# Optimization experiments

Measured on AMD Instinct MI355X. Metric: run time of the kernel, lower is better.

The kernel has to match this reference:

```python
import jax, jax.numpy as jnp
import numpy as np

HIDDEN = 4096
FFN = 14336
GS = 64  # groupsize


def dequant2(qw, scales, zeros, N):
    """Unpack 2-bit HQQ weights. qw: (N//4, K) int32, scales/zeros: (G, K).
    Returns W of shape (N, K) float: (bits - zeros[n % G]) * scales[n % G]."""
    G = scales.shape[0]
    n = jnp.arange(N)
    packed = qw[n // 4]                      # (N, K)
    shift = ((3 - (n % 4)) * 2).astype(qw.dtype)  # per-row bit shift
    vals = (packed >> shift[:, None]) & 3    # (N, K) 2-bit codes
    g = n % G
    return (vals.astype(scales.dtype) - zeros[g]) * scales[g]


def setup_inputs() -> dict:
    key = jax.random.key(0)
    ks = jax.random.split(key, 12)
    x = jax.random.normal(ks[0], (512, HIDDEN), dtype=jnp.float32)
    qw1 = jax.random.randint(ks[1], (FFN // 4, HIDDEN), 0, 256, dtype=jnp.int32)
    qw3 = jax.random.randint(ks[2], (FFN // 4, HIDDEN), 0, 256, dtype=jnp.int32)
    qw2 = jax.random.randint(ks[3], (HIDDEN // 4, FFN), 0, 256, dtype=jnp.int32)
    G1 = FFN // GS
    G2 = HIDDEN // GS
    s1 = jax.random.uniform(ks[4], (G1, HIDDEN), dtype=jnp.float32) * 0.05
    z1 = jax.random.uniform(ks[5], (G1, HIDDEN), dtype=jnp.float32)
    s3 = jax.random.uniform(ks[6], (G1, HIDDEN), dtype=jnp.float32) * 0.05
    z3 = jax.random.uniform(ks[7], (G1, HIDDEN), dtype=jnp.float32)
    s2 = jax.random.uniform(ks[8], (G2, FFN), dtype=jnp.float32) * 0.05
    z2 = jax.random.uniform(ks[9], (G2, FFN), dtype=jnp.float32)
    return {"x": x, "qw1": qw1, "s1": s1, "z1": z1, "qw3": qw3, "s3": s3,
            "z3": z3, "qw2": qw2, "s2": s2, "z2": z2, "groupsize": GS}


def reference(x, qw1, s1, z1, qw3, s3, z3, qw2, s2, z2, groupsize):
    # gate / up projections: C = x @ W^T, W dequantized to (N, K)
    w1 = dequant2(qw1, s1, z1, FFN)      # (FFN, HIDDEN)
    w3 = dequant2(qw3, s3, z3, FFN)      # (FFN, HIDDEN)
    w2 = dequant2(qw2, s2, z2, HIDDEN)   # (HIDDEN, FFN)
    gate = jnp.einsum('mk,nk->mn', x, w1)   # (M, FFN)
    up = jnp.einsum('mk,nk->mn', x, w3)     # (M, FFN)
    h = jax.nn.silu(gate) * up               # SwiGLU
    out = jnp.einsum('mf,hf->mh', h, w2)     # (M, HIDDEN)
    return out
```

## Files before the change

### kernel.cpp

```cpp
#include <hip/hip_runtime.h>
#include <hip/hip_fp16.h>
#include <stdint.h>

#define HIDDEN 4096
#define FFN    14336
#define MDIM   512
#define G1     224
#define G2     64
#define BK     64
#define KB_H   128
#define KB_F   448

typedef _Float16 f16x8 __attribute__((ext_vector_type(8)));
typedef float f32x4 __attribute__((ext_vector_type(4)));

#define SCHED0() __builtin_amdgcn_sched_barrier(0);
#define LGKM_BAR()                                            \
    asm volatile("s_waitcnt lgkmcnt(0)" ::: "memory");        \
    __builtin_amdgcn_s_barrier();                             \
    __builtin_amdgcn_sched_barrier(0);

__global__ void prep_fused(const float* __restrict__ x,
                           const float* __restrict__ s1, const float* __restrict__ z1,
                           const float* __restrict__ s3, const float* __restrict__ z3,
                           const float* __restrict__ s2, const float* __restrict__ z2,
                           ushort* __restrict__ xbp, uint32_t* __restrict__ szp1,
                           uint32_t* __restrict__ szp3, uint32_t* __restrict__ szp2,
                           float* __restrict__ out) {
    const int b = blockIdx.x, t = threadIdx.x;
    if (b < 1024) {
        int i = b * 256 + t;
        int ls = i & 63;
        int kb = (i >> 6) & (KB_H - 1);
        int mb = i >> 13;
        int row = mb * 16 + (ls & 15);
        int col = kb * 32 + (ls >> 4) * 8;
        const float4* src = (const float4*)&x[(size_t)row * HIDDEN + col];
        float4 v0 = src[0], v1 = src[1];
        __half2 h0 = __floats2half2_rn(v0.x, v0.y);
        __half2 h1 = __floats2half2_rn(v0.z, v0.w);
        __half2 h2 = __floats2half2_rn(v1.x, v1.y);
        __half2 h3 = __floats2half2_rn(v1.z, v1.w);
        ((uint4*)xbp)[i] = make_uint4(
            __builtin_bit_cast(uint32_t, h0), __builtin_bit_cast(uint32_t, h1),
            __builtin_bit_cast(uint32_t, h2), __builtin_bit_cast(uint32_t, h3));
    } else if (b < 6400) {
        const int seg = (b - 1024) / 1792;
        const int i = (b - 1024 - seg * 1792) * 256 + t;
        const float* sp = (seg == 0) ? s1 : (seg == 1) ? s3 : s2;
        const float* zp = (seg == 0) ? z1 : (seg == 1) ? z3 : z2;
        uint32_t* op = (seg == 0) ? szp1 : (seg == 1) ? szp3 : szp2;
        float sv0 = sp[2 * i], sv1 = sp[2 * i + 1];
        float zv0 = zp[2 * i], zv1 = zp[2 * i + 1];
        __half2 hs = __floats2half2_rn(sv0, sv1);
        __half2 hn = __floats2half2_rn(-zv0 * sv0, -zv1 * sv1);
        ((uint2*)op)[i] = make_uint2(__builtin_bit_cast(uint32_t, hs),
                                     __builtin_bit_cast(uint32_t, hn));
    } else {
        int i = (b - 6400) * 256 + t;
        ((float4*)out)[i] = make_float4(0.f, 0.f, 0.f, 0.f);
    }
}

__device__ __forceinline__ uint32_t deq2(uint32_t w0, uint32_t w1, uint32_t sh,
                                         uint32_t spair, uint32_t npair) {
    uint32_t c0 = (w0 >> sh) & 3u;
    uint32_t c1 = (w1 >> sh) & 3u;
    uint32_t sel = 0x01000100u + c0 * 0x0202u + c1 * 0x02020000u;
    uint32_t codes = __builtin_amdgcn_perm(0x42004000u, 0x3C000000u, sel);
    __half2 r = __hfma2(__builtin_bit_cast(__half2, codes),
                        __builtin_bit_cast(__half2, spair),
                        __builtin_bit_cast(__half2, npair));
    return __builtin_bit_cast(uint32_t, r);
}


__global__ __launch_bounds__(256, 2)
void gemm_gateup(const ushort* __restrict__ xbp, const uint32_t* __restrict__ qw1,
                 const uint32_t* __restrict__ sz1, const uint32_t* __restrict__ qw3,
                 const uint32_t* __restrict__ sz3, ushort* __restrict__ hp) {
    __shared__ ushort sB1[2][32 * 64];
    __shared__ ushort sB2[2][32 * 64];
    __shared__ ushort sE[256 * 32];

    const int tid = threadIdx.x;
    const int idx = ((blockIdx.x & 7) * 112) + (blockIdx.x >> 3);
    const int mt = idx & 1, nt = idx >> 1;
    const int m0 = mt * 256, n0 = nt * 32;

    const int lane = tid & 63, w = tid >> 6;
    const int wm = w * 64;
    const int frow = lane & 15, fk = (lane >> 4) * 8;
    const int sw = (frow & 7) << 3;

    uint32_t abase[4];
#pragma unroll
    for (int mi = 0; mi < 4; ++mi)
        abase[mi] = (uint32_t)(((m0 >> 4) + w * 4 + mi) * KB_H) * 512 + lane * 8;

    const int bi = tid & 127;
    const int rp = bi >> 3;
    const int kc = (bi & 7) * 8;
    const int row0 = rp * 2;
    const int g0 = (n0 + row0) % G1;
    const uint32_t* qp = (tid < 128 ? qw1 : qw3) + (size_t)(n0 / 4 + (rp >> 1)) * HIDDEN + kc;
    const uint32_t* zp = (tid < 128 ? sz1 : sz3) + (size_t)g0 * HIDDEN + kc;
    ushort (*sB)[32 * 64] = (tid < 128) ? sB1 : sB2;
    const uint32_t sh0 = 6u - 4u * (uint32_t)(rp & 1);

    f32x4 accG[4][2], accU[4][2];
#pragma unroll
    for (int i = 0; i < 4; ++i)
#pragma unroll
        for (int j = 0; j < 2; ++j) {
            accG[i][j] = (f32x4){0.f, 0.f, 0.f, 0.f};
            accU[i][j] = (f32x4){0.f, 0.f, 0.f, 0.f};
        }

    f16x8 afA[8], afB[8];
    uint4 pwA0, pwA1, pzA0, pzA1, pzA2, pzA3;
    uint4 pwB0, pwB1, pzB0, pzB1, pzB2, pzB3;

#define GU_LDA(AF, tt)                                                         \
    { _Pragma("unroll")                                                        \
      for (int mi = 0; mi < 4; ++mi)                                           \
          _Pragma("unroll")                                                    \
          for (int kk = 0; kk < 2; ++kk)                                       \
              AF[mi * 2 + kk] =                                                \
                  *(const f16x8*)&xbp[abase[mi] + (uint32_t)((tt) * 2 + kk) * 512]; }

#define GU_LD(PW0, PW1, PZ0, PZ1, PZ2, PZ3, k0q)                               \
    PW0 = *(const uint4*)(qp + (k0q));                                         \
    PW1 = *(const uint4*)(qp + (k0q) + 4);                                     \
    PZ0 = *(const uint4*)(zp + (k0q));                                         \
    PZ1 = *(const uint4*)(zp + (k0q) + 4);                                     \
    PZ2 = *(const uint4*)(zp + HIDDEN + (k0q));                                \
    PZ3 = *(const uint4*)(zp + HIDDEN + (k0q) + 4);

#define GU_DEQ(wbuf, PW0, PW1, PZ0, PZ1, PZ2, PZ3)                             \
    { const uint32_t wv[8] = {(PW0).x, (PW0).y, (PW0).z, (PW0).w,              \
                              (PW1).x, (PW1).y, (PW1).z, (PW1).w};             \
      {   const uint32_t sp[4] = {(PZ0).x, (PZ0).z, (PZ1).x, (PZ1).z};         \
          const uint32_t np[4] = {(PZ0).y, (PZ0).w, (PZ1).y, (PZ1).w};         \
          uint32_t o[4];                                                       \
          _Pragma("unroll")                                                    \
          for (int j = 0; j < 4; ++j)                                          \
              o[j] = deq2(wv[2*j], wv[2*j+1], sh0, sp[j], np[j]);              \
          *(uint4*)&sB[wbuf][row0 * 64 + (kc ^ ((row0 & 7) << 3))] =           \
              make_uint4(o[0], o[1], o[2], o[3]);                              \
      }                                                                        \
      {   const uint32_t sp[4] = {(PZ2).x, (PZ2).z, (PZ3).x, (PZ3).z};         \
          const uint32_t np[4] = {(PZ2).y, (PZ2).w, (PZ3).y, (PZ3).w};         \
          uint32_t o[4];                                                       \
          _Pragma("unroll")                                                    \
          for (int j = 0; j < 4; ++j)                                          \
              o[j] = deq2(wv[2*j], wv[2*j+1], sh0 - 2u, sp[j], np[j]);         \
          const int row1 = row0 + 1;                                           \
          *(uint4*)&sB[wbuf][row1 * 64 + (kc ^ ((row1 & 7) << 3))] =           \
              make_uint4(o[0], o[1], o[2], o[3]);                              \
      } }

#define GU_COMP(AF, rbuf)                                                      \
    { _Pragma("unroll")                                                        \
      for (int kk = 0; kk < 2; ++kk) {                                         \
          const int col = ((kk * 32) + fk) ^ sw;                               \
          f16x8 bg0 = *(const f16x8*)&sB1[rbuf][frow * 64 + col];              \
          f16x8 bg1 = *(const f16x8*)&sB1[rbuf][(16 + frow) * 64 + col];       \
          f16x8 bu0 = *(const f16x8*)&sB2[rbuf][frow * 64 + col];              \
          f16x8 bu1 = *(const f16x8*)&sB2[rbuf][(16 + frow) * 64 + col];       \
          _Pragma("unroll")                                                    \
          for (int mi = 0; mi < 4; ++mi) {                                     \
              accG[mi][0] = __builtin_amdgcn_mfma_f32_16x16x32_f16(AF[mi*2+kk], bg0, accG[mi][0], 0, 0, 0); \
              accG[mi][1] = __builtin_amdgcn_mfma_f32_16x16x32_f16(AF[mi*2+kk], bg1, accG[mi][1], 0, 0, 0); \
              accU[mi][0] = __builtin_amdgcn_mfma_f32_16x16x32_f16(AF[mi*2+kk], bu0, accU[mi][0], 0, 0, 0); \
              accU[mi][1] = __builtin_amdgcn_mfma_f32_16x16x32_f16(AF[mi*2+kk], bu1, accU[mi][1], 0, 0, 0); \
          } } }

#define GU_STEP(tcur, AFW, AFR, WBUF, RBUF, PW0, PW1, PZ0, PZ1, PZ2, PZ3, DOLDA, DOLQ) \
    { if (DOLDA) { GU_LDA(AFW, (tcur) + 1) } SCHED0()                          \
      GU_DEQ(WBUF, PW0, PW1, PZ0, PZ1, PZ2, PZ3)                               \
      if (DOLQ) { GU_LD(PW0, PW1, PZ0, PZ1, PZ2, PZ3, ((tcur) + 3) * BK) }     \
      GU_COMP(AFR, RBUF)                                                       \
      LGKM_BAR() }

    GU_LD(pwA0, pwA1, pzA0, pzA1, pzA2, pzA3, 0)
    GU_LDA(afA, 0)
    GU_DEQ(0, pwA0, pwA1, pzA0, pzA1, pzA2, pzA3)
    GU_LD(pwA0, pwA1, pzA0, pzA1, pzA2, pzA3, BK)
    GU_LD(pwB0, pwB1, pzB0, pzB1, pzB2, pzB3, 2 * BK)
    LGKM_BAR()

    for (int t = 0; t < 60; t += 2) {
        GU_STEP(t,     afB, afA, 1, 0, pwA0, pwA1, pzA0, pzA1, pzA2, pzA3, 1, 1)
        GU_STEP(t + 1, afA, afB, 0, 1, pwB0, pwB1, pzB0, pzB1, pzB2, pzB3, 1, 1)
    }
    GU_STEP(60, afB, afA, 1, 0, pwA0, pwA1, pzA0, pzA1, pzA2, pzA3, 1, 1)
    GU_STEP(61, afA, afB, 0, 1, pwB0, pwB1, pzB0, pzB1, pzB2, pzB3, 1, 0)
    GU_STEP(62, afB, afA, 1, 0, pwA0, pwA1, pzA0, pzA1, pzA2, pzA3, 1, 0)
    GU_COMP(afB, 1)

    const int rb = (lane >> 4) * 4, cb = lane & 15;
#pragma unroll
    for (int mi = 0; mi < 4; ++mi)
#pragma unroll
        for (int ni = 0; ni < 2; ++ni) {
            f32x4 g = accG[mi][ni], u = accU[mi][ni];
            const int row = wm + mi * 16 + rb;
            const int colx = ni * 16 + cb;
#pragma unroll
            for (int r = 0; r < 4; ++r) {
                float gv = g[r];
                float hv = __fdividef(gv, 1.0f + __expf(-gv)) * u[r];
                __half hh = __float2half(hv);
                sE[(row + r) * 32 + colx] = __builtin_bit_cast(ushort, hh);
            }
        }
    __syncthreads();
    {
#pragma unroll
        for (int j = 0; j < 4; ++j) {
            const int slot = tid + j * 256;
            const int mbi = slot >> 6, ls = slot & 63;
            uint4 v = *(const uint4*)&sE[(mbi * 16 + (ls & 15)) * 32 + (ls >> 4) * 8];
            *(uint4*)&hp[(size_t)(((m0 >> 4) + mbi) * KB_F + nt) * 512 + ls * 8] = v;
        }
    }
#undef GU_LDA
#undef GU_LD
#undef GU_DEQ
#undef GU_COMP
#undef GU_STEP
}


__global__ __launch_bounds__(256, 2)
void gemm_down(const ushort* __restrict__ hp, const uint32_t* __restrict__ qw2,
               const uint32_t* __restrict__ sz2, float* __restrict__ out) {
    __shared__ ushort sBd[2][32 * 64];

    const int tid = threadIdx.x;
    const int idx = ((blockIdx.x & 7) * 64) + (blockIdx.x >> 3);
    const int mt = idx & 1, nt = (idx >> 1) & 127, sk = idx >> 8;
    const int m0 = mt * 256, n0 = nt * 32;
    const int kb0 = sk * 224;
    const int kbeg = sk * (FFN / 2);

    const int lane = tid & 63, w = tid >> 6;
    const int wm = w * 64;
    const int frow = lane & 15, fk = (lane >> 4) * 8;
    const int sw = (frow & 7) << 3;

    uint32_t abase[4];
#pragma unroll
    for (int mi = 0; mi < 4; ++mi)
        abase[mi] = (uint32_t)(((m0 >> 4) + w * 4 + mi) * KB_F + kb0) * 512 + lane * 8;

    const int r = tid >> 3;
    const int kc = (tid & 7) * 8;
    const int g = ((nt & 1) * 32) + r;
    const uint32_t* qp = qw2 + (size_t)(n0 / 4 + (r >> 2)) * FFN + kbeg + kc;
    const uint32_t* zp = sz2 + (size_t)g * FFN + kbeg + kc;
    const uint32_t sh = 6u - 2u * (uint32_t)(r & 3);

    f32x4 acc[4][2];
#pragma unroll
    for (int i = 0; i < 4; ++i)
#pragma unroll
        for (int j = 0; j < 2; ++j) acc[i][j] = (f32x4){0.f, 0.f, 0.f, 0.f};

    f16x8 afA[8], afB[8];
    uint4 pwA0, pwA1, pzA0, pzA1;
    uint4 pwB0, pwB1, pzB0, pzB1;

#define GD_LDA(AF, tt)                                                         \
    { _Pragma("unroll")                                                        \
      for (int mi = 0; mi < 4; ++mi)                                           \
          _Pragma("unroll")                                                    \
          for (int kk = 0; kk < 2; ++kk)                                       \
              AF[mi * 2 + kk] =                                                \
                  *(const f16x8*)&hp[abase[mi] + (uint32_t)((tt) * 2 + kk) * 512]; }

#define GD_LD(PW0, PW1, PZ0, PZ1, k0q)                                         \
    PW0 = *(const uint4*)(qp + (k0q));                                         \
    PW1 = *(const uint4*)(qp + (k0q) + 4);                                     \
    PZ0 = *(const uint4*)(zp + (k0q));                                         \
    PZ1 = *(const uint4*)(zp + (k0q) + 4);

#define GD_DEQ(wbuf, PW0, PW1, PZ0, PZ1)                                       \
    { const uint32_t wv[8] = {(PW0).x, (PW0).y, (PW0).z, (PW0).w,              \
                              (PW1).x, (PW1).y, (PW1).z, (PW1).w};             \
      const uint32_t sp[4] = {(PZ0).x, (PZ0).z, (PZ1).x, (PZ1).z};             \
      const uint32_t np[4] = {(PZ0).y, (PZ0).w, (PZ1).y, (PZ1).w};             \
      uint32_t o[4];                                                           \
      _Pragma("unroll")                                                        \
      for (int j = 0; j < 4; ++j)                                              \
          o[j] = deq2(wv[2*j], wv[2*j+1], sh, sp[j], np[j]);                   \
      *(uint4*)&sBd[wbuf][r * 64 + (kc ^ ((r & 7) << 3))] =                    \
          make_uint4(o[0], o[1], o[2], o[3]); }

#define GD_COMP(AF, rbuf)                                                      \
    { _Pragma("unroll")                                                        \
      for (int kk = 0; kk < 2; ++kk) {                                         \
          const int col = ((kk * 32) + fk) ^ sw;                               \
          f16x8 bf0 = *(const f16x8*)&sBd[rbuf][frow * 64 + col];              \
          f16x8 bf1 = *(const f16x8*)&sBd[rbuf][(16 + frow) * 64 + col];       \
          _Pragma("unroll")                                                    \
          for (int mi = 0; mi < 4; ++mi) {                                     \
              acc[mi][0] = __builtin_amdgcn_mfma_f32_16x16x32_f16(AF[mi*2+kk], bf0, acc[mi][0], 0, 0, 0); \
              acc[mi][1] = __builtin_amdgcn_mfma_f32_16x16x32_f16(AF[mi*2+kk], bf1, acc[mi][1], 0, 0, 0); \
          } } }

#define GD_STEP(tcur, AFW, AFR, WBUF, RBUF, PW0, PW1, PZ0, PZ1, DOLDA, DOLQ)   \
    { if (DOLDA) { GD_LDA(AFW, (tcur) + 1) } SCHED0()                          \
      GD_DEQ(WBUF, PW0, PW1, PZ0, PZ1)                                         \
      if (DOLQ) { GD_LD(PW0, PW1, PZ0, PZ1, ((tcur) + 3) * BK) }               \
      GD_COMP(AFR, RBUF)                                                       \
      LGKM_BAR() }

    GD_LD(pwA0, pwA1, pzA0, pzA1, 0)
    GD_LDA(afA, 0)
    GD_DEQ(0, pwA0, pwA1, pzA0, pzA1)
    GD_LD(pwA0, pwA1, pzA0, pzA1, BK)
    GD_LD(pwB0, pwB1, pzB0, pzB1, 2 * BK)
    LGKM_BAR()

    for (int t = 0; t < 108; t += 2) {
        GD_STEP(t,     afB, afA, 1, 0, pwA0, pwA1, pzA0, pzA1, 1, 1)
        GD_STEP(t + 1, afA, afB, 0, 1, pwB0, pwB1, pzB0, pzB1, 1, 1)
    }
    GD_STEP(108, afB, afA, 1, 0, pwA0, pwA1, pzA0, pzA1, 1, 1)
    GD_STEP(109, afA, afB, 0, 1, pwB0, pwB1, pzB0, pzB1, 1, 0)
    GD_STEP(110, afB, afA, 1, 0, pwA0, pwA1, pzA0, pzA1, 1, 0)
    GD_COMP(afB, 1)

    const int rb = (lane >> 4) * 4, cb = lane & 15;
#pragma unroll
    for (int mi = 0; mi < 4; ++mi)
#pragma unroll
        for (int ni = 0; ni < 2; ++ni) {
            f32x4 a = acc[mi][ni];
            const int mm = m0 + wm + mi * 16 + rb;
            const int nn = n0 + ni * 16 + cb;
#pragma unroll
            for (int rr = 0; rr < 4; ++rr)
                atomicAdd(&out[(size_t)(mm + rr) * HIDDEN + nn], a[rr]);
        }
#undef GD_LDA
#undef GD_LD
#undef GD_DEQ
#undef GD_COMP
#undef GD_STEP
}


extern "C" void kernel_launch(void* const* d_in, const int* in_sizes, int n_in,
                              void* d_out, int out_size, void* d_ws, size_t ws_size,
                              hipStream_t stream) {
    (void)in_sizes; (void)n_in; (void)out_size; (void)ws_size;

    const float* x  = (const float*)d_in[0];
    const uint32_t* qw1 = (const uint32_t*)d_in[1];
    const float* s1 = (const float*)d_in[2];
    const float* z1 = (const float*)d_in[3];
    const uint32_t* qw3 = (const uint32_t*)d_in[4];
    const float* s3 = (const float*)d_in[5];
    const float* z3 = (const float*)d_in[6];
    const uint32_t* qw2 = (const uint32_t*)d_in[7];
    const float* s2 = (const float*)d_in[8];
    const float* z2 = (const float*)d_in[9];
    float* out = (float*)d_out;

    char* ws = (char*)d_ws;
    ushort*   xbp  = (ushort*)ws;
    uint32_t* szp1 = (uint32_t*)(ws + (size_t)MDIM * HIDDEN * 2);
    uint32_t* szp3 = szp1 + (size_t)G1 * HIDDEN;
    uint32_t* szp2 = szp3 + (size_t)G1 * HIDDEN;
    ushort*   hp   = (ushort*)(szp2 + (size_t)G2 * FFN);

    prep_fused<<<8448, 256, 0, stream>>>(x, s1, z1, s3, z3, s2, z2,
                                         xbp, szp1, szp3, szp2, out);
    gemm_gateup<<<(FFN / 32) * (MDIM / 256), 256, 0, stream>>>(xbp, qw1, szp1, qw3, szp3, hp);
    gemm_down<<<2 * (MDIM / 256) * (HIDDEN / 32), 256, 0, stream>>>(hp, qw2, szp2, out);
}
```

Measured before the change: 293.1 us.

## Cover full M per gate/up block and replace split-K atomics with partial-sum reduce

The gate/up kernel now processes all 512 rows per block instead of 256. Each B tile is dequantized once rather than twice, and the grid is halved to 448 blocks, with twice the accumulator registers per wave. Its pipeline is restructured: A fragments load in even/odd halves interleaved with MFMAs, only one set of prefetch registers is kept, and MFMA sections run at raised priority. The down projection writes split-K partial sums to a workspace and a new reduce kernel adds them, replacing float atomics and the output zeroing in prep. This costs an extra launch and more memory traffic.

```diff
diff --git a/kernel.cpp b/kernel.cpp
--- a/kernel.cpp
+++ b/kernel.cpp
@@ -25,8 +25,7 @@
                            const float* __restrict__ s3, const float* __restrict__ z3,
                            const float* __restrict__ s2, const float* __restrict__ z2,
                            ushort* __restrict__ xbp, uint32_t* __restrict__ szp1,
-                           uint32_t* __restrict__ szp3, uint32_t* __restrict__ szp2,
-                           float* __restrict__ out) {
+                           uint32_t* __restrict__ szp3, uint32_t* __restrict__ szp2) {
     const int b = blockIdx.x, t = threadIdx.x;
     if (b < 1024) {
         int i = b * 256 + t;
@@ -44,7 +43,7 @@
         ((uint4*)xbp)[i] = make_uint4(
             __builtin_bit_cast(uint32_t, h0), __builtin_bit_cast(uint32_t, h1),
             __builtin_bit_cast(uint32_t, h2), __builtin_bit_cast(uint32_t, h3));
-    } else if (b < 6400) {
+    } else {
         const int seg = (b - 1024) / 1792;
         const int i = (b - 1024 - seg * 1792) * 256 + t;
         const float* sp = (seg == 0) ? s1 : (seg == 1) ? s3 : s2;
@@ -56,9 +55,6 @@
         __half2 hn = __floats2half2_rn(-zv0 * sv0, -zv1 * sv1);
         ((uint2*)op)[i] = make_uint2(__builtin_bit_cast(uint32_t, hs),
                                      __builtin_bit_cast(uint32_t, hn));
-    } else {
-        int i = (b - 6400) * 256 + t;
-        ((float4*)out)[i] = make_float4(0.f, 0.f, 0.f, 0.f);
     }
 }
 
@@ -81,22 +77,21 @@
                  const uint32_t* __restrict__ sz3, ushort* __restrict__ hp) {
     __shared__ ushort sB1[2][32 * 64];
     __shared__ ushort sB2[2][32 * 64];
-    __shared__ ushort sE[256 * 32];
+    __shared__ ushort sE[512 * 32];
 
     const int tid = threadIdx.x;
-    const int idx = ((blockIdx.x & 7) * 112) + (blockIdx.x >> 3);
-    const int mt = idx & 1, nt = idx >> 1;
-    const int m0 = mt * 256, n0 = nt * 32;
+    const int nt = ((blockIdx.x & 7) * 56) + (blockIdx.x >> 3);
+    const int n0 = nt * 32;
 
     const int lane = tid & 63, w = tid >> 6;
-    const int wm = w * 64;
+    const int wm = w * 128;
     const int frow = lane & 15, fk = (lane >> 4) * 8;
     const int sw = (frow & 7) << 3;
 
-    uint32_t abase[4];
-#pragma unroll
-    for (int mi = 0; mi < 4; ++mi)
-        abase[mi] = (uint32_t)(((m0 >> 4) + w * 4 + mi) * KB_H) * 512 + lane * 8;
+    uint32_t abase[8];
+#pragma unroll
+    for (int mi = 0; mi < 8; ++mi)
+        abase[mi] = (uint32_t)((w * 8 + mi) * KB_H) * 512 + lane * 8;
 
     const int bi = tid & 127;
     const int rp = bi >> 3;
@@ -107,101 +102,97 @@
     const uint32_t* zp = (tid < 128 ? sz1 : sz3) + (size_t)g0 * HIDDEN + kc;
     ushort (*sB)[32 * 64] = (tid < 128) ? sB1 : sB2;
     const uint32_t sh0 = 6u - 4u * (uint32_t)(rp & 1);
-
-    f32x4 accG[4][2], accU[4][2];
-#pragma unroll
-    for (int i = 0; i < 4; ++i)
+    const int wc0 = row0 * 64 + (kc ^ ((row0 & 7) << 3));
+    const int wc1 = (row0 + 1) * 64 + (kc ^ (((row0 + 1) & 7) << 3));
+
+    f32x4 accG[8][2], accU[8][2];
+#pragma unroll
+    for (int i = 0; i < 8; ++i)
 #pragma unroll
         for (int j = 0; j < 2; ++j) {
             accG[i][j] = (f32x4){0.f, 0.f, 0.f, 0.f};
             accU[i][j] = (f32x4){0.f, 0.f, 0.f, 0.f};
         }
 
-    f16x8 afA[8], afB[8];
-    uint4 pwA0, pwA1, pzA0, pzA1, pzA2, pzA3;
-    uint4 pwB0, pwB1, pzB0, pzB1, pzB2, pzB3;
-
-#define GU_LDA(AF, tt)                                                         \
+    f16x8 afE[8], afO[8];
+    uint4 pw0, pw1, pz0, pz1, pz2, pz3;
+
+#define GU_LDAE(tt)                                                            \
     { _Pragma("unroll")                                                        \
-      for (int mi = 0; mi < 4; ++mi)                                           \
-          _Pragma("unroll")                                                    \
-          for (int kk = 0; kk < 2; ++kk)                                       \
-              AF[mi * 2 + kk] =                                                \
-                  *(const f16x8*)&xbp[abase[mi] + (uint32_t)((tt) * 2 + kk) * 512]; }
-
-#define GU_LD(PW0, PW1, PZ0, PZ1, PZ2, PZ3, k0q)                               \
-    PW0 = *(const uint4*)(qp + (k0q));                                         \
-    PW1 = *(const uint4*)(qp + (k0q) + 4);                                     \
-    PZ0 = *(const uint4*)(zp + (k0q));                                         \
-    PZ1 = *(const uint4*)(zp + (k0q) + 4);                                     \
-    PZ2 = *(const uint4*)(zp + HIDDEN + (k0q));                                \
-    PZ3 = *(const uint4*)(zp + HIDDEN + (k0q) + 4);
-
-#define GU_DEQ(wbuf, PW0, PW1, PZ0, PZ1, PZ2, PZ3)                             \
-    { const uint32_t wv[8] = {(PW0).x, (PW0).y, (PW0).z, (PW0).w,              \
-                              (PW1).x, (PW1).y, (PW1).z, (PW1).w};             \
-      {   const uint32_t sp[4] = {(PZ0).x, (PZ0).z, (PZ1).x, (PZ1).z};         \
-          const uint32_t np[4] = {(PZ0).y, (PZ0).w, (PZ1).y, (PZ1).w};         \
+      for (int mi = 0; mi < 8; ++mi)                                           \
+          afE[mi] = *(const f16x8*)&xbp[abase[mi] + (uint32_t)((tt) * 2) * 512]; }
+
+#define GU_LDAO(tt)                                                            \
+    { _Pragma("unroll")                                                        \
+      for (int mi = 0; mi < 8; ++mi)                                           \
+          afO[mi] = *(const f16x8*)&xbp[abase[mi] + (uint32_t)((tt) * 2 + 1) * 512]; }
+
+#define GU_LDQZ(k0q)                                                           \
+    pw0 = *(const uint4*)(qp + (k0q));                                         \
+    pw1 = *(const uint4*)(qp + (k0q) + 4);                                     \
+    pz0 = *(const uint4*)(zp + (k0q));                                         \
+    pz1 = *(const uint4*)(zp + (k0q) + 4);                                     \
+    pz2 = *(const uint4*)(zp + HIDDEN + (k0q));                                \
+    pz3 = *(const uint4*)(zp + HIDDEN + (k0q) + 4);
+
+#define GU_DEQ(wbuf)                                                           \
+    { const uint32_t wv[8] = {pw0.x, pw0.y, pw0.z, pw0.w,                      \
+                              pw1.x, pw1.y, pw1.z, pw1.w};                     \
+      {   const uint32_t sp[4] = {pz0.x, pz0.z, pz1.x, pz1.z};                 \
+          const uint32_t np[4] = {pz0.y, pz0.w, pz1.y, pz1.w};                 \
           uint32_t o[4];                                                       \
           _Pragma("unroll")                                                    \
           for (int j = 0; j < 4; ++j)                                          \
               o[j] = deq2(wv[2*j], wv[2*j+1], sh0, sp[j], np[j]);              \
-          *(uint4*)&sB[wbuf][row0 * 64 + (kc ^ ((row0 & 7) << 3))] =           \
-              make_uint4(o[0], o[1], o[2], o[3]);                              \
+          *(uint4*)&sB[wbuf][wc0] = make_uint4(o[0], o[1], o[2], o[3]);        \
       }                                                                        \
-      {   const uint32_t sp[4] = {(PZ2).x, (PZ2).z, (PZ3).x, (PZ3).z};         \
-          const uint32_t np[4] = {(PZ2).y, (PZ2).w, (PZ3).y, (PZ3).w};         \
+      {   const uint32_t sp[4] = {pz2.x, pz2.z, pz3.x, pz3.z};                 \
+          const uint32_t np[4] = {pz2.y, pz2.w, pz3.y, pz3.w};                 \
           uint32_t o[4];                                                       \
           _Pragma("unroll")                                                    \
           for (int j = 0; j < 4; ++j)                                          \
               o[j] = deq2(wv[2*j], wv[2*j+1], sh0 - 2u, sp[j], np[j]);         \
-          const int row1 = row0 + 1;                                           \
-          *(uint4*)&sB[wbuf][row1 * 64 + (kc ^ ((row1 & 7) << 3))] =           \
-              make_uint4(o[0], o[1], o[2], o[3]);                              \
+          *(uint4*)&sB[wbuf][wc1] = make_uint4(o[0], o[1], o[2], o[3]);        \
       } }
 
-#define GU_COMP(AF, rbuf)                                                      \
-    { _Pragma("unroll")                                                        \
-      for (int kk = 0; kk < 2; ++kk) {                                         \
-          const int col = ((kk * 32) + fk) ^ sw;                               \
-          f16x8 bg0 = *(const f16x8*)&sB1[rbuf][frow * 64 + col];              \
-          f16x8 bg1 = *(const f16x8*)&sB1[rbuf][(16 + frow) * 64 + col];       \
-          f16x8 bu0 = *(const f16x8*)&sB2[rbuf][frow * 64 + col];              \
-          f16x8 bu1 = *(const f16x8*)&sB2[rbuf][(16 + frow) * 64 + col];       \
-          _Pragma("unroll")                                                    \
-          for (int mi = 0; mi < 4; ++mi) {                                     \
-              accG[mi][0] = __builtin_amdgcn_mfma_f32_16x16x32_f16(AF[mi*2+kk], bg0, accG[mi][0], 0, 0, 0); \
-              accG[mi][1] = __builtin_amdgcn_mfma_f32_16x16x32_f16(AF[mi*2+kk], bg1, accG[mi][1], 0, 0, 0); \
-              accU[mi][0] = __builtin_amdgcn_mfma_f32_16x16x32_f16(AF[mi*2+kk], bu0, accU[mi][0], 0, 0, 0); \
-              accU[mi][1] = __builtin_amdgcn_mfma_f32_16x16x32_f16(AF[mi*2+kk], bu1, accU[mi][1], 0, 0, 0); \
-          } } }
-
-#define GU_STEP(tcur, AFW, AFR, WBUF, RBUF, PW0, PW1, PZ0, PZ1, PZ2, PZ3, DOLDA, DOLQ) \
-    { if (DOLDA) { GU_LDA(AFW, (tcur) + 1) } SCHED0()                          \
-      GU_DEQ(WBUF, PW0, PW1, PZ0, PZ1, PZ2, PZ3)                               \
-      if (DOLQ) { GU_LD(PW0, PW1, PZ0, PZ1, PZ2, PZ3, ((tcur) + 3) * BK) }     \
-      GU_COMP(AFR, RBUF)                                                       \
-      LGKM_BAR() }
-
-    GU_LD(pwA0, pwA1, pzA0, pzA1, pzA2, pzA3, 0)
-    GU_LDA(afA, 0)
-    GU_DEQ(0, pwA0, pwA1, pzA0, pzA1, pzA2, pzA3)
-    GU_LD(pwA0, pwA1, pzA0, pzA1, pzA2, pzA3, BK)
-    GU_LD(pwB0, pwB1, pzB0, pzB1, pzB2, pzB3, 2 * BK)
+#define GU_MFMA(AF, rbuf, kk)                                                  \
+    { const int col = ((kk) * 32 + fk) ^ sw;                                   \
+      f16x8 bg0 = *(const f16x8*)&sB1[rbuf][frow * 64 + col];                  \
+      f16x8 bg1 = *(const f16x8*)&sB1[rbuf][(16 + frow) * 64 + col];           \
+      f16x8 bu0 = *(const f16x8*)&sB2[rbuf][frow * 64 + col];                  \
+      f16x8 bu1 = *(const f16x8*)&sB2[rbuf][(16 + frow) * 64 + col];           \
+      __builtin_amdgcn_s_setprio(1);                                           \
+      _Pragma("unroll")                                                        \
+      for (int mi = 0; mi < 8; ++mi) {                                         \
+          accG[mi][0] = __builtin_amdgcn_mfma_f32_16x16x32_f16(AF[mi], bg0, accG[mi][0], 0, 0, 0); \
+          accG[mi][1] = __builtin_amdgcn_mfma_f32_16x16x32_f16(AF[mi], bg1, accG[mi][1], 0, 0, 0); \
+          accU[mi][0] = __builtin_amdgcn_mfma_f32_16x16x32_f16(AF[mi], bu0, accU[mi][0], 0, 0, 0); \
+          accU[mi][1] = __builtin_amdgcn_mfma_f32_16x16x32_f16(AF[mi], bu1, accU[mi][1], 0, 0, 0); \
+      }                                                                        \
+      __builtin_amdgcn_s_setprio(0); }
+
+    GU_LDQZ(0)
+    GU_LDAE(0)
+    GU_LDAO(0)
+    GU_DEQ(0)
+    GU_LDQZ(BK)
     LGKM_BAR()
 
-    for (int t = 0; t < 60; t += 2) {
-        GU_STEP(t,     afB, afA, 1, 0, pwA0, pwA1, pzA0, pzA1, pzA2, pzA3, 1, 1)
-        GU_STEP(t + 1, afA, afB, 0, 1, pwB0, pwB1, pzB0, pzB1, pzB2, pzB3, 1, 1)
+    for (int t = 0; t < 63; ++t) {
+        GU_DEQ((t + 1) & 1)
+        if (t < 62) { GU_LDQZ((t + 2) * BK) }
+        GU_MFMA(afE, t & 1, 0)
+        GU_LDAE(t + 1)
+        GU_MFMA(afO, t & 1, 1)
+        GU_LDAO(t + 1)
+        LGKM_BAR()
     }
-    GU_STEP(60, afB, afA, 1, 0, pwA0, pwA1, pzA0, pzA1, pzA2, pzA3, 1, 1)
-    GU_STEP(61, afA, afB, 0, 1, pwB0, pwB1, pzB0, pzB1, pzB2, pzB3, 1, 0)
-    GU_STEP(62, afB, afA, 1, 0, pwA0, pwA1, pzA0, pzA1, pzA2, pzA3, 1, 0)
-    GU_COMP(afB, 1)
+    GU_MFMA(afE, 1, 0)
+    GU_MFMA(afO, 1, 1)
 
     const int rb = (lane >> 4) * 4, cb = lane & 15;
 #pragma unroll
-    for (int mi = 0; mi < 4; ++mi)
+    for (int mi = 0; mi < 8; ++mi)
 #pragma unroll
         for (int ni = 0; ni < 2; ++ni) {
             f32x4 g = accG[mi][ni], u = accU[mi][ni];
@@ -218,24 +209,24 @@
     __syncthreads();
     {
 #pragma unroll
-        for (int j = 0; j < 4; ++j) {
+        for (int j = 0; j < 8; ++j) {
             const int slot = tid + j * 256;
             const int mbi = slot >> 6, ls = slot & 63;
             uint4 v = *(const uint4*)&sE[(mbi * 16 + (ls & 15)) * 32 + (ls >> 4) * 8];
-            *(uint4*)&hp[(size_t)(((m0 >> 4) + mbi) * KB_F + nt) * 512 + ls * 8] = v;
+            *(uint4*)&hp[(size_t)(mbi * KB_F + nt) * 512 + ls * 8] = v;
         }
     }
-#undef GU_LDA
-#undef GU_LD
+#undef GU_LDAE
+#undef GU_LDAO
+#undef GU_LDQZ
 #undef GU_DEQ
-#undef GU_COMP
-#undef GU_STEP
+#undef GU_MFMA
 }
 
 
 __global__ __launch_bounds__(256, 2)
 void gemm_down(const ushort* __restrict__ hp, const uint32_t* __restrict__ qw2,
-               const uint32_t* __restrict__ sz2, float* __restrict__ out) {
+               const uint32_t* __restrict__ sz2, float* __restrict__ part) {
     __shared__ ushort sBd[2][32 * 64];
 
     const int tid = threadIdx.x;
@@ -333,6 +324,7 @@
     GD_STEP(110, afB, afA, 1, 0, pwA0, pwA1, pzA0, pzA1, 1, 0)
     GD_COMP(afB, 1)
 
+    float* pp = part + (size_t)sk * MDIM * HIDDEN;
     const int rb = (lane >> 4) * 4, cb = lane & 15;
 #pragma unroll
     for (int mi = 0; mi < 4; ++mi)
@@ -342,14 +334,24 @@
             const int mm = m0 + wm + mi * 16 + rb;
             const int nn = n0 + ni * 16 + cb;
 #pragma unroll
-            for (int rr = 0; rr < 4; ++rr)
-                atomicAdd(&out[(size_t)(mm + rr) * HIDDEN + nn], a[rr]);
+            for (int rr = 0; rr < 4; ++rr) pp[(size_t)(mm + rr) * HIDDEN + nn] = a[rr];
         }
 #undef GD_LDA
 #undef GD_LD
 #undef GD_DEQ
 #undef GD_COMP
 #undef GD_STEP
+}
+
+
+__global__ void reduce_out(const float* __restrict__ part, float* __restrict__ out) {
+    int i = blockIdx.x * blockDim.x + threadIdx.x;
+    const int Q = MDIM * HIDDEN / 4;
+    float4 a = ((const float4*)part)[i];
+    float4 b = ((const float4*)part)[i + Q];
+    float4 o;
+    o.x = a.x + b.x; o.y = a.y + b.y; o.z = a.z + b.z; o.w = a.w + b.w;
+    ((float4*)out)[i] = o;
 }
 
 
@@ -376,9 +378,11 @@
     uint32_t* szp3 = szp1 + (size_t)G1 * HIDDEN;
     uint32_t* szp2 = szp3 + (size_t)G1 * HIDDEN;
     ushort*   hp   = (ushort*)(szp2 + (size_t)G2 * FFN);
-
-    prep_fused<<<8448, 256, 0, stream>>>(x, s1, z1, s3, z3, s2, z2,
-                                         xbp, szp1, szp3, szp2, out);
-    gemm_gateup<<<(FFN / 32) * (MDIM / 256), 256, 0, stream>>>(xbp, qw1, szp1, qw3, szp3, hp);
-    gemm_down<<<2 * (MDIM / 256) * (HIDDEN / 32), 256, 0, stream>>>(hp, qw2, szp2, out);
-}
+    float*    part = (float*)((char*)hp + (size_t)MDIM * FFN * 2);
+
+    prep_fused<<<6400, 256, 0, stream>>>(x, s1, z1, s3, z3, s2, z2,
+                                         xbp, szp1, szp3, szp2);
+    gemm_gateup<<<FFN / 32, 256, 0, stream>>>(xbp, qw1, szp1, qw3, szp3, hp);
+    gemm_down<<<2 * (MDIM / 256) * (HIDDEN / 32), 256, 0, stream>>>(hp, qw2, szp2, part);
+    reduce_out<<<(MDIM * HIDDEN / 4) / 256, 256, 0, stream>>>(part, out);
+}
```

Result: slower. 377.5 us (+28.8%).
